# Performance work log

Hardware: AMD Instinct MI355X
Metric: run time of the kernel (lower is better)

Reference implementation:

```python
import jax, jax.numpy as jnp
import numpy as np

B, N, T, D, H = 64, 207, 24, 128, 8
DK = D // H
EPS = 1e-5


def setup_inputs() -> dict:
    key = jax.random.key(0)
    ks = jax.random.split(key, 18)
    s = 1.0 / np.sqrt(D)
    inp = {
        "hidden": jax.random.normal(ks[0], (B, N, T, D), jnp.float32),
        "matrix": jax.random.uniform(ks[1], (B, T, N, N), jnp.float32) / N,
        "Wq": jax.random.normal(ks[2], (D, D), jnp.float32) * s,
        "bq": jnp.zeros((D,), jnp.float32),
        "Wk": jax.random.normal(ks[3], (D, D), jnp.float32) * s,
        "bk": jnp.zeros((D,), jnp.float32),
        "Wv": jax.random.normal(ks[4], (D, D), jnp.float32) * s,
        "bv": jnp.zeros((D,), jnp.float32),
        "Wo": jax.random.normal(ks[5], (D, D), jnp.float32) * s,
        "bo": jnp.zeros((D,), jnp.float32),
        "Wgcn": jax.random.normal(ks[6], (D, D), jnp.float32) * s,
        "bgcn": jnp.zeros((D,), jnp.float32),
        "Wgate": jax.random.normal(ks[7], (D, 2 * D), jnp.float32) * (1.0 / np.sqrt(2 * D)),
        "bgate": jnp.zeros((D,), jnp.float32),
        "gamma": jnp.ones((D,), jnp.float32),
        "beta": jnp.zeros((D,), jnp.float32),
    }
    return inp


def reference(hidden, matrix, Wq, bq, Wk, bk, Wv, bv, Wo, bo,
              Wgcn, bgcn, Wgate, bgate, gamma, beta):
    # ---- GCN branch: per-timestep A·X then channel mixing (dmodel->dmodel)
    # hidden: [B,N,T,D], matrix: [B,T,N,N] -> aggregated [B,N,T,D]
    agg = jnp.einsum('bntc,btnm->bmtc', hidden, matrix)
    gcn_out = agg @ Wgcn.T + bgcn                       # [B,N,T,D]

    # ---- Causal multi-head temporal attention
    q = (hidden @ Wq.T + bq).reshape(B, N, T, H, DK)
    k = (hidden @ Wk.T + bk).reshape(B, N, T, H, DK)
    v = (hidden @ Wv.T + bv).reshape(B, N, T, H, DK)
    scale = 1.0 / np.sqrt(DK)
    scores = jnp.einsum('bnthe,bnshe->bnhts', q, k)     # [B,N,H,T,T]
    causal = jnp.triu(jnp.ones((T, T), bool), k=1)      # mask future
    scores = jnp.where(causal, -jnp.inf, scores)
    attn = jax.nn.softmax(scale * scores, axis=-1)
    ctx = jnp.einsum('bnhts,bnshd->bnthd', attn, v).reshape(B, N, T, D)
    attn_out = ctx @ Wo.T + bo                          # [B,N,T,D]

    # ---- Gated fusion: concat -> linear -> batchnorm (training stats) -> sigmoid
    gate_in = jnp.concatenate([gcn_out, attn_out], axis=-1)  # [B,N,T,2D]
    g = gate_in @ Wgate.T + bgate                            # [B,N,T,D]
    mean = jnp.mean(g, axis=(0, 1, 2))
    var = jnp.var(g, axis=(0, 1, 2))
    g = (g - mean) * jax.lax.rsqrt(var + EPS) * gamma + beta
    z = jax.nn.sigmoid(g)
    return z * gcn_out + (1.0 - z) * attn_out
```

## Files before the change

kernel.cpp:

```cpp
#include <hip/hip_runtime.h>

#define B_ 64
#define N_ 207
#define T_ 24
#define D_ 128
#define H_ 8
#define MROWS (B_*N_*T_)
#define SELEMS ((size_t)MROWS * D_)
#define NBLK_FB 768
#define BNROWS_FB 414
#define NBLK_FUSED (MROWS/128)
#define EPS_ 1e-5f

typedef __attribute__((ext_vector_type(8))) short s16x8;
typedef __attribute__((ext_vector_type(4))) float f32x4;

#define MFMA16(a,b,c) __builtin_amdgcn_mfma_f32_16x16x32_bf16(a,b,c,0,0,0)

__device__ __forceinline__ float bfu2f(unsigned short u) {
  return __uint_as_float(((unsigned int)u) << 16);
}
__device__ __forceinline__ unsigned short f2bfu(float f) {
  unsigned int x = __float_as_uint(f);
  return (unsigned short)((x + 0x7fffu + ((x >> 16) & 1u)) >> 16);
}
__device__ __forceinline__ unsigned int packbf2(float lo, float hi) {
  return (unsigned int)f2bfu(lo) | ((unsigned int)f2bfu(hi) << 16);
}

__global__ __launch_bounds__(256) void k_wcast(
    const float* __restrict__ Wq, const float* __restrict__ Wk,
    const float* __restrict__ Wv, const float* __restrict__ Wo,
    const float* __restrict__ Wgcn, const float* __restrict__ Wgate,
    unsigned short* __restrict__ out)
{
  const int idx4 = (blockIdx.x * 256 + threadIdx.x) * 4;
  if (idx4 >= 114688) return;
  const float* src; int off;
  if      (idx4 < 16384) { src = Wq;    off = idx4; }
  else if (idx4 < 32768) { src = Wk;    off = idx4 - 16384; }
  else if (idx4 < 49152) { src = Wv;    off = idx4 - 32768; }
  else if (idx4 < 65536) { src = Wo;    off = idx4 - 49152; }
  else if (idx4 < 81920) { src = Wgcn;  off = idx4 - 65536; }
  else                   { src = Wgate; off = idx4 - 81920; }
  const float4 v = *(const float4*)(src + off);
  ushort4 u;
  u.x = f2bfu(v.x); u.y = f2bfu(v.y); u.z = f2bfu(v.z); u.w = f2bfu(v.w);
  *(ushort4*)(out + idx4) = u;
}

__device__ __forceinline__ void gcn_load(
    const float* __restrict__ mbase, const float* __restrict__ hbase,
    int m0, int nn, int cb, int ch,
    float va[8], float vb[8], float ha[8], float hb[8])
{
  const int n_r0 = ch*32 + nn, n_r1 = n_r0 + 1;
  const bool rv0 = (n_r0 < N_), rv1 = (n_r1 < N_);
  const size_t nc0 = (size_t)(rv0 ? n_r0 : 0);
  const size_t nc1 = (size_t)(rv1 ? n_r1 : 0);
  {
    const float* r0 = mbase + nc0*N_ + m0 + cb;
    const float* r1 = mbase + nc1*N_ + m0 + cb;
    #pragma unroll
    for (int j = 0; j < 2; ++j) {
      const int mg = m0 + cb + j*4;
      if (mg + 3 < N_) {
        const float4 x0 = *(const float4*)(r0 + j*4);
        const float4 x1 = *(const float4*)(r1 + j*4);
        va[j*4+0]=x0.x; va[j*4+1]=x0.y; va[j*4+2]=x0.z; va[j*4+3]=x0.w;
        vb[j*4+0]=x1.x; vb[j*4+1]=x1.y; vb[j*4+2]=x1.z; vb[j*4+3]=x1.w;
      } else {
        #pragma unroll
        for (int e = 0; e < 4; ++e) {
          const bool ok = (mg + e) < N_;
          va[j*4+e] = ok ? r0[j*4+e] : 0.f;
          vb[j*4+e] = ok ? r1[j*4+e] : 0.f;
        }
      }
    }
    #pragma unroll
    for (int e = 0; e < 8; ++e) {
      if (!rv0) va[e] = 0.f;
      if (!rv1) vb[e] = 0.f;
    }
  }
  {
    const float* r0 = hbase + nc0*(T_*D_) + cb;
    const float* r1 = hbase + nc1*(T_*D_) + cb;
    const float4 x0a = *(const float4*)(r0);
    const float4 x0b = *(const float4*)(r0 + 4);
    const float4 x1a = *(const float4*)(r1);
    const float4 x1b = *(const float4*)(r1 + 4);
    ha[0]=x0a.x; ha[1]=x0a.y; ha[2]=x0a.z; ha[3]=x0a.w;
    ha[4]=x0b.x; ha[5]=x0b.y; ha[6]=x0b.z; ha[7]=x0b.w;
    hb[0]=x1a.x; hb[1]=x1a.y; hb[2]=x1a.z; hb[3]=x1a.w;
    hb[4]=x1b.x; hb[5]=x1b.y; hb[6]=x1b.z; hb[7]=x1b.w;
    #pragma unroll
    for (int e = 0; e < 8; ++e) {
      if (!rv0) ha[e] = 0.f;
      if (!rv1) hb[e] = 0.f;
    }
  }
}

__global__ __launch_bounds__(256) void k_gcn2(
    const float* __restrict__ hidden, const float* __restrict__ matrix,
    const unsigned short* __restrict__ Wgcnb, const float* __restrict__ bgcn,
    unsigned short* __restrict__ gcn)
{
  __shared__ __align__(16) unsigned char smem[40960];
  unsigned short* GsAll = (unsigned short*)smem;

  const int tid = threadIdx.x;
  const int w = tid >> 6, l = tid & 63;
  const int lr = l & 15, lg = l >> 4;
  const int m0 = blockIdx.x * 128;
  const int by = (int)blockIdx.y;
  const int b = by / T_, t = by % T_;

  const int nn = (tid & 15) * 2;
  const int cb = (tid >> 4) * 8;

  const float* mbase = matrix + (size_t)(b*T_ + t)*N_*N_;
  const float* hbase = hidden + (size_t)b*N_*T_*D_ + (size_t)t*D_;

  f32x4 acc1[2][8];
  #pragma unroll
  for (int mt = 0; mt < 2; mt++)
    #pragma unroll
    for (int nt = 0; nt < 8; nt++)
      #pragma unroll
      for (int e = 0; e < 4; e++) acc1[mt][nt][e] = 0.f;

  float va[8], vb[8], ha[8], hb[8];
  gcn_load(mbase, hbase, m0, nn, cb, 0, va, vb, ha, hb);

  #pragma unroll
  for (int ch = 0; ch < 7; ++ch) {
    unsigned char* base = smem + ((ch & 1) ? 20480 : 0);
    unsigned int* M32 = (unsigned int*)base;
    unsigned int* H32 = (unsigned int*)(base + 10240);
    #pragma unroll
    for (int e = 0; e < 8; ++e)
      M32[(cb + e)*20 + (tid & 15)] = packbf2(va[e], vb[e]);
    #pragma unroll
    for (int e = 0; e < 8; ++e)
      H32[(cb + e)*20 + (tid & 15)] = packbf2(ha[e], hb[e]);
    if (ch < 6)
      gcn_load(mbase, hbase, m0, nn, cb, ch + 1, va, vb, ha, hb);
    __syncthreads();
    const unsigned short* M16 = (const unsigned short*)M32;
    const unsigned short* H16 = (const unsigned short*)H32;
    const s16x8 af0 = *(const s16x8*)(M16 + (size_t)(w*32 +  0 + lr)*40 + lg*8);
    const s16x8 af1 = *(const s16x8*)(M16 + (size_t)(w*32 + 16 + lr)*40 + lg*8);
    #pragma unroll
    for (int nt = 0; nt < 8; ++nt) {
      const s16x8 bf = *(const s16x8*)(H16 + (size_t)(nt*16 + lr)*40 + lg*8);
      acc1[0][nt] = MFMA16(af0, bf, acc1[0][nt]);
      acc1[1][nt] = MFMA16(af1, bf, acc1[1][nt]);
    }
  }

  __syncthreads();
  unsigned short* gs = GsAll + (size_t)w * (32*136);
  #pragma unroll
  for (int nt = 0; nt < 8; nt++)
    #pragma unroll
    for (int mt = 0; mt < 2; mt++)
      #pragma unroll
      for (int r = 0; r < 4; r++)
        gs[(mt*16 + lg*4 + r)*136 + nt*16 + lr] = f2bfu(acc1[mt][nt][r]);

  f32x4 acc2[2][8];
  #pragma unroll
  for (int mt = 0; mt < 2; mt++)
    #pragma unroll
    for (int nt = 0; nt < 8; nt++)
      #pragma unroll
      for (int e = 0; e < 4; e++) acc2[mt][nt][e] = 0.f;

  #pragma unroll
  for (int ks = 0; ks < 4; ++ks) {
    const s16x8 a0 = *(const s16x8*)(gs + (size_t)( 0 + lr)*136 + ks*32 + lg*8);
    const s16x8 a1 = *(const s16x8*)(gs + (size_t)(16 + lr)*136 + ks*32 + lg*8);
    #pragma unroll
    for (int nt = 0; nt < 8; ++nt) {
      const s16x8 bf = *(const s16x8*)(Wgcnb + (size_t)(nt*16 + lr)*D_ + ks*32 + lg*8);
      acc2[0][nt] = MFMA16(a0, bf, acc2[0][nt]);
      acc2[1][nt] = MFMA16(a1, bf, acc2[1][nt]);
    }
  }

  #pragma unroll
  for (int nt = 0; nt < 8; nt++) {
    const float bsc = bgcn[nt*16 + lr];
    #pragma unroll
    for (int mt = 0; mt < 2; mt++)
      #pragma unroll
      for (int r = 0; r < 4; r++)
        gs[(mt*16 + lg*4 + r)*136 + nt*16 + lr] = f2bfu(acc2[mt][nt][r] + bsc);
  }
  const size_t Obase = ((size_t)b*N_ + (m0 + w*32))*(size_t)(T_*D_) + (size_t)t*D_;
  #pragma unroll
  for (int p = 0; p < 8; p++) {
    const int c = p*64 + l;
    const int row = c >> 4, c8 = (c & 15) * 8;
    const int gm = m0 + w*32 + row;
    if (gm < N_) {
      const s16x8 v = *(const s16x8*)(gs + row*136 + c8);
      *(s16x8*)(gcn + Obase + (size_t)row*(T_*D_) + c8) = v;
    }
  }
}

__global__ __launch_bounds__(256) void k_attn3(
    const float* __restrict__ hidden,
    const unsigned short* __restrict__ Wqb, const unsigned short* __restrict__ Wkb,
    const unsigned short* __restrict__ Wvb, const unsigned short* __restrict__ Wob,
    const float* __restrict__ bq, const float* __restrict__ bk,
    const float* __restrict__ bv, const float* __restrict__ bo,
    unsigned short* __restrict__ attnO)
{
  __shared__ __align__(16) unsigned short Xs[32*136], Qs[32*136],
                                          Ks[32*136], Vs[32*136];
  const int tid = threadIdx.x;
  const int w = tid >> 6, l = tid & 63;
  const int lr = l & 15, lg = l >> 4;
  const size_t bn = blockIdx.x;
  const float* X = hidden + bn * (size_t)(T_*D_);

  for (int i = tid; i < 32*16; i += 256) {
    const int row = i >> 4, g8 = (i & 15) * 8;
    s16x8 v;
    if (row < T_) {
      const float4 a  = *(const float4*)(X + (size_t)row*D_ + g8);
      const float4 b2 = *(const float4*)(X + (size_t)row*D_ + g8 + 4);
      v[0]=(short)f2bfu(a.x);  v[1]=(short)f2bfu(a.y);
      v[2]=(short)f2bfu(a.z);  v[3]=(short)f2bfu(a.w);
      v[4]=(short)f2bfu(b2.x); v[5]=(short)f2bfu(b2.y);
      v[6]=(short)f2bfu(b2.z); v[7]=(short)f2bfu(b2.w);
    } else {
      #pragma unroll
      for (int e = 0; e < 8; e++) v[e] = 0;
    }
    *(s16x8*)&Xs[row*136 + g8] = v;
  }
  __syncthreads();

  s16x8 af[2][4];
  #pragma unroll
  for (int mt = 0; mt < 2; mt++)
    #pragma unroll
    for (int ks = 0; ks < 4; ks++)
      af[mt][ks] = *(const s16x8*)&Xs[(mt*16 + lr)*136 + ks*32 + lg*8];

  const unsigned short* Wp[3] = {Wqb, Wkb, Wvb};
  const float*          bp[3] = {bq, bk, bv};
  unsigned short*       Op[3] = {Qs, Ks, Vs};
  #pragma unroll
  for (int o = 0; o < 3; o++) {
    f32x4 acc[2][2];
    #pragma unroll
    for (int mt = 0; mt < 2; mt++)
      #pragma unroll
      for (int nt = 0; nt < 2; nt++)
        #pragma unroll
        for (int e = 0; e < 4; e++) acc[mt][nt][e] = 0.f;
    #pragma unroll
    for (int ks = 0; ks < 4; ks++) {
      #pragma unroll
      for (int nt = 0; nt < 2; nt++) {
        const s16x8 bf = *(const s16x8*)(Wp[o] + (size_t)(w*32 + nt*16 + lr)*D_ + ks*32 + lg*8);
        acc[0][nt] = MFMA16(af[0][ks], bf, acc[0][nt]);
        acc[1][nt] = MFMA16(af[1][ks], bf, acc[1][nt]);
      }
    }
    #pragma unroll
    for (int nt = 0; nt < 2; nt++) {
      const float bb = bp[o][w*32 + nt*16 + lr];
      #pragma unroll
      for (int mt = 0; mt < 2; mt++)
        #pragma unroll
        for (int r = 0; r < 4; r++)
          Op[o][(mt*16 + lg*4 + r)*136 + w*32 + nt*16 + lr] =
              f2bfu(acc[mt][nt][r] + bb);
    }
  }
  __syncthreads();

  if (tid < H_*T_) {
    const int h = tid / T_, t = tid % T_;
    const int hb = h * 16;
    float q[16];
    {
      const s16x8 q0 = *(const s16x8*)&Qs[t*136 + hb];
      const s16x8 q1 = *(const s16x8*)&Qs[t*136 + hb + 8];
      #pragma unroll
      for (int e = 0; e < 8; e++) {
        q[e]   = bfu2f((unsigned short)q0[e]);
        q[8+e] = bfu2f((unsigned short)q1[e]);
      }
    }
    float p[T_];
    float mx = -1e30f;
    #pragma unroll
    for (int s = 0; s < T_; s++) {
      const s16x8 k0 = *(const s16x8*)&Ks[s*136 + hb];
      const s16x8 k1 = *(const s16x8*)&Ks[s*136 + hb + 8];
      float d = 0.f;
      #pragma unroll
      for (int e = 0; e < 8; e++) {
        d += q[e]   * bfu2f((unsigned short)k0[e]);
        d += q[8+e] * bfu2f((unsigned short)k1[e]);
      }
      d *= 0.25f;
      d = (s <= t) ? d : -1e30f;
      p[s] = d;
      mx = fmaxf(mx, d);
    }
    float den = 0.f;
    #pragma unroll
    for (int s = 0; s < T_; s++) {
      float e = __expf(p[s] - mx);
      e = (s <= t) ? e : 0.f;
      p[s] = e;
      den += e;
    }
    const float rd = 1.f / den;
    float o[16];
    #pragma unroll
    for (int e = 0; e < 16; e++) o[e] = 0.f;
    #pragma unroll
    for (int s = 0; s < T_; s++) {
      const float ps = p[s];
      const s16x8 v0 = *(const s16x8*)&Vs[s*136 + hb];
      const s16x8 v1 = *(const s16x8*)&Vs[s*136 + hb + 8];
      #pragma unroll
      for (int e = 0; e < 8; e++) {
        o[e]   += ps * bfu2f((unsigned short)v0[e]);
        o[8+e] += ps * bfu2f((unsigned short)v1[e]);
      }
    }
    s16x8 r0, r1;
    #pragma unroll
    for (int e = 0; e < 8; e++) {
      r0[e] = (short)f2bfu(o[e]   * rd);
      r1[e] = (short)f2bfu(o[8+e] * rd);
    }
    *(s16x8*)&Qs[t*136 + hb]     = r0;
    *(s16x8*)&Qs[t*136 + hb + 8] = r1;
  }
  __syncthreads();

  s16x8 cf[2][4];
  #pragma unroll
  for (int mt = 0; mt < 2; mt++)
    #pragma unroll
    for (int ks = 0; ks < 4; ks++)
      cf[mt][ks] = *(const s16x8*)&Qs[(mt*16 + lr)*136 + ks*32 + lg*8];
  f32x4 acc2[2][2];
  #pragma unroll
  for (int mt = 0; mt < 2; mt++)
    #pragma unroll
    for (int nt = 0; nt < 2; nt++)
      #pragma unroll
      for (int e = 0; e < 4; e++) acc2[mt][nt][e] = 0.f;
  #pragma unroll
  for (int ks = 0; ks < 4; ks++) {
    #pragma unroll
    for (int nt = 0; nt < 2; nt++) {
      const s16x8 bf = *(const s16x8*)(Wob + (size_t)(w*32 + nt*16 + lr)*D_ + ks*32 + lg*8);
      acc2[0][nt] = MFMA16(cf[0][ks], bf, acc2[0][nt]);
      acc2[1][nt] = MFMA16(cf[1][ks], bf, acc2[1][nt]);
    }
  }
  #pragma unroll
  for (int nt = 0; nt < 2; nt++) {
    const float bb = bo[w*32 + nt*16 + lr];
    #pragma unroll
    for (int mt = 0; mt < 2; mt++)
      #pragma unroll
      for (int r = 0; r < 4; r++)
        Xs[(mt*16 + lg*4 + r)*136 + w*32 + nt*16 + lr] =
            f2bfu(acc2[mt][nt][r] + bb);
  }
  __syncthreads();
  unsigned short* O = attnO + bn * (size_t)(T_*D_);
  for (int i = tid; i < 24*16; i += 256) {
    const int row = i >> 4, g8 = (i & 15) * 8;
    *(s16x8*)(O + (size_t)row*D_ + g8) = *(const s16x8*)&Xs[row*136 + g8];
  }
}

template<bool STATS>
__global__ __launch_bounds__(256) void k_gate(
    const unsigned short* __restrict__ A0, const unsigned short* __restrict__ A1,
    const unsigned short* __restrict__ Wb, const float* __restrict__ bias,
    float* __restrict__ Out, float* __restrict__ psum, float* __restrict__ psq)
{
  __shared__ float lbs[4*128], lbq[4*128];
  const int tid = threadIdx.x;
  const int w = tid >> 6, l = tid & 63;
  const int lr = l & 15, lg = l >> 4;
  const size_t m0 = (size_t)blockIdx.x * 128 + w * 32;

  f32x4 acc[2][8];
  #pragma unroll
  for (int mt = 0; mt < 2; mt++)
    #pragma unroll
    for (int nt = 0; nt < 8; nt++)
      #pragma unroll
      for (int e = 0; e < 4; e++) acc[mt][nt][e] = 0.f;

  #pragma unroll
  for (int ks = 0; ks < 8; ks++) {
    const unsigned short* Asrc = (ks >= 4) ? A1 : A0;
    const int kk = (ks >= 4) ? ks - 4 : ks;
    const s16x8 a0 = *(const s16x8*)(Asrc + (m0 +  0 + lr)*D_ + kk*32 + lg*8);
    const s16x8 a1 = *(const s16x8*)(Asrc + (m0 + 16 + lr)*D_ + kk*32 + lg*8);
    #pragma unroll
    for (int nt = 0; nt < 8; nt++) {
      const s16x8 bf = *(const s16x8*)(Wb + (size_t)(nt*16 + lr)*256 + ks*32 + lg*8);
      acc[0][nt] = MFMA16(a0, bf, acc[0][nt]);
      acc[1][nt] = MFMA16(a1, bf, acc[1][nt]);
    }
  }

  #pragma unroll
  for (int nt = 0; nt < 8; nt++) {
    const float b = bias[nt*16 + lr];
    float s = 0.f, q = 0.f;
    #pragma unroll
    for (int mt = 0; mt < 2; mt++)
      #pragma unroll
      for (int r = 0; r < 4; r++) {
        const float v = acc[mt][nt][r] + b;
        Out[(m0 + mt*16 + lg*4 + r)*D_ + nt*16 + lr] = v;
        if (STATS) { s += v; q += v*v; }
      }
    if (STATS) {
      s += __shfl_xor(s, 16); s += __shfl_xor(s, 32);
      q += __shfl_xor(q, 16); q += __shfl_xor(q, 32);
      if (lg == 0) {
        lbs[w*128 + nt*16 + lr] = s;
        lbq[w*128 + nt*16 + lr] = q;
      }
    }
  }
  if (STATS) {
    __syncthreads();
    if (tid < 128) {
      const float ss = lbs[tid] + lbs[128 + tid] + lbs[256 + tid] + lbs[384 + tid];
      const float qq = lbq[tid] + lbq[128 + tid] + lbq[256 + tid] + lbq[384 + tid];
      psum[(size_t)blockIdx.x*128 + tid] = ss;
      psq [(size_t)blockIdx.x*128 + tid] = qq;
    }
  }
}

__global__ __launch_bounds__(256) void k_bnstats(
    const float* __restrict__ g, float* __restrict__ psum, float* __restrict__ psq)
{
  const int tid = threadIdx.x;
  const int c4 = (tid & 31) * 4, sub = tid >> 5;
  const size_t r0 = (size_t)blockIdx.x * BNROWS_FB;
  float4 s = make_float4(0.f,0.f,0.f,0.f), q = make_float4(0.f,0.f,0.f,0.f);
  for (int i = sub; i < BNROWS_FB; i += 8) {
    const float4 x = *(const float4*)(g + (r0 + i)*D_ + c4);
    s.x += x.x; s.y += x.y; s.z += x.z; s.w += x.w;
    q.x += x.x*x.x; q.y += x.y*x.y; q.z += x.z*x.z; q.w += x.w*x.w;
  }
  __shared__ float ls[8*128], lq[8*128];
  *(float4*)&ls[sub*128 + c4] = s;
  *(float4*)&lq[sub*128 + c4] = q;
  __syncthreads();
  if (tid < 128) {
    float ss = 0.f, qq = 0.f;
    #pragma unroll
    for (int k = 0; k < 8; k++) { ss += ls[k*128 + tid]; qq += lq[k*128 + tid]; }
    psum[(size_t)blockIdx.x*128 + tid] = ss;
    psq [(size_t)blockIdx.x*128 + tid] = qq;
  }
}

__global__ __launch_bounds__(1024) void k_bnfinal(
    const float* __restrict__ psum, const float* __restrict__ psq, int nblk,
    float* __restrict__ meanv, float* __restrict__ invstdv)
{
  const int tid = threadIdx.x;
  const int sub = tid >> 7, ch = tid & 127;
  float s = 0.f, q = 0.f;
  for (int i = sub; i < nblk; i += 8) {
    s += psum[(size_t)i*128 + ch];
    q += psq [(size_t)i*128 + ch];
  }
  __shared__ float ls[8*128], lq[8*128];
  ls[sub*128 + ch] = s; lq[sub*128 + ch] = q;
  __syncthreads();
  if (tid < 128) {
    float ss = 0.f, qq = 0.f;
    #pragma unroll
    for (int k = 0; k < 8; k++) { ss += ls[k*128 + tid]; qq += lq[k*128 + tid]; }
    const float mean = ss / (float)MROWS;
    const float var  = qq / (float)MROWS - mean*mean;
    meanv[tid] = mean;
    invstdv[tid] = rsqrtf(var + EPS_);
  }
}

__global__ __launch_bounds__(256) void k_final(
    float* __restrict__ g,
    const unsigned short* __restrict__ gcn, const unsigned short* __restrict__ attn,
    const float* __restrict__ meanv, const float* __restrict__ invstdv,
    const float* __restrict__ gamma, const float* __restrict__ beta)
{
  const size_t tot4 = SELEMS >> 2;
  for (size_t i4 = (size_t)blockIdx.x*blockDim.x + threadIdx.x; i4 < tot4;
       i4 += (size_t)gridDim.x*blockDim.x) {
    const int c4 = (int)(i4 & 31) * 4;
    const float4 gv = ((const float4*)g)[i4];
    const ushort4 gc = ((const ushort4*)gcn)[i4];
    const ushort4 at = ((const ushort4*)attn)[i4];
    const float4 m4 = *(const float4*)(meanv + c4);
    const float4 s4 = *(const float4*)(invstdv + c4);
    const float4 ga = *(const float4*)(gamma + c4);
    const float4 be = *(const float4*)(beta + c4);
    float4 outv;
    { const float y = (gv.x - m4.x)*s4.x*ga.x + be.x;
      const float z = 1.f/(1.f + __expf(-y));
      outv.x = z*bfu2f(gc.x) + (1.f - z)*bfu2f(at.x); }
    { const float y = (gv.y - m4.y)*s4.y*ga.y + be.y;
      const float z = 1.f/(1.f + __expf(-y));
      outv.y = z*bfu2f(gc.y) + (1.f - z)*bfu2f(at.y); }
    { const float y = (gv.z - m4.z)*s4.z*ga.z + be.z;
      const float z = 1.f/(1.f + __expf(-y));
      outv.z = z*bfu2f(gc.z) + (1.f - z)*bfu2f(at.z); }
    { const float y = (gv.w - m4.w)*s4.w*ga.w + be.w;
      const float z = 1.f/(1.f + __expf(-y));
      outv.w = z*bfu2f(gc.w) + (1.f - z)*bfu2f(at.w); }
    ((float4*)g)[i4] = outv;
  }
}

extern "C" void kernel_launch(void* const* d_in, const int* in_sizes, int n_in,
                              void* d_out, int out_size, void* d_ws, size_t ws_size,
                              hipStream_t stream)
{
  (void)in_sizes; (void)n_in; (void)out_size;
  const float* hidden = (const float*)d_in[0];
  const float* matrix = (const float*)d_in[1];
  const float* Wq   = (const float*)d_in[2];  const float* bq    = (const float*)d_in[3];
  const float* Wk   = (const float*)d_in[4];  const float* bk    = (const float*)d_in[5];
  const float* Wv   = (const float*)d_in[6];  const float* bv    = (const float*)d_in[7];
  const float* Wo   = (const float*)d_in[8];  const float* bo    = (const float*)d_in[9];
  const float* Wgcn = (const float*)d_in[10]; const float* bgcn  = (const float*)d_in[11];
  const float* Wgate= (const float*)d_in[12]; const float* bgate = (const float*)d_in[13];
  const float* gamma= (const float*)d_in[14]; const float* beta  = (const float*)d_in[15];
  float* out = (float*)d_out;

  unsigned short* WB = (unsigned short*)d_ws;
  unsigned short* Wqb    = WB;
  unsigned short* Wkb    = WB + 16384;
  unsigned short* Wvb    = WB + 32768;
  unsigned short* Wob    = WB + 49152;
  unsigned short* Wgcnb  = WB + 65536;
  unsigned short* Wgateb = WB + 81920;
  unsigned short* X1     = WB + 114688;
  unsigned short* X2     = X1 + SELEMS;
  float* psum    = (float*)(X2 + SELEMS);

  const size_t base_bytes = (size_t)(WB + 114688 - (unsigned short*)d_ws)*2
                          + 2*SELEMS*2;
  const size_t fused_bytes = base_bytes + ((size_t)NBLK_FUSED*128*2 + 256)*4;
  const bool fused = (ws_size >= fused_bytes);
  const int nblk = fused ? NBLK_FUSED : NBLK_FB;
  float* psq     = psum + (size_t)nblk*128;
  float* meanv   = psq  + (size_t)nblk*128;
  float* invstdv = meanv + 128;

  k_wcast<<<112, 256, 0, stream>>>(Wq, Wk, Wv, Wo, Wgcn, Wgate, WB);
  k_gcn2 <<<dim3(2, B_*T_), 256, 0, stream>>>(hidden, matrix, Wgcnb, bgcn, X2);
  k_attn3<<<B_*N_, 256, 0, stream>>>(hidden, Wqb, Wkb, Wvb, Wob,
                                     bq, bk, bv, bo, X1);
  if (fused) {
    k_gate<true><<<MROWS/128, 256, 0, stream>>>(X2, X1, Wgateb, bgate, out, psum, psq);
  } else {
    k_gate<false><<<MROWS/128, 256, 0, stream>>>(X2, X1, Wgateb, bgate, out, psum, psq);
    k_bnstats<<<NBLK_FB, 256, 0, stream>>>(out, psum, psq);
  }
  k_bnfinal<<<1, 1024, 0, stream>>>(psum, psq, nblk, meanv, invstdv);
  k_final<<<2048, 256, 0, stream>>>(out, X2, X1, meanv, invstdv, gamma, beta);
}
```

Baseline: 815.6 us.

## Compute causal attention scores and PV with per-wave MFMA instead of scalar loops

Replaces the scalar per-thread attention (192 threads each looping over 24 keys) with MFMA tiles. Each wave computes QK^T and P·V for the two heads whose columns it produced in the projection, so no block barrier is needed between projection and attention. V is stored transposed in shared memory and the probabilities are staged in a per-wave buffer as bf16. The softmax now skips max subtraction and rounds probabilities to bf16, which trades some numerical robustness for speed.

New measurement: 750.9 us. -7.9%, faster.

```diff
diff --git a/kernel.cpp b/kernel.cpp
--- a/kernel.cpp
+++ b/kernel.cpp
@@ -221,8 +221,11 @@
     const float* __restrict__ bv, const float* __restrict__ bo,
     unsigned short* __restrict__ attnO)
 {
-  __shared__ __align__(16) unsigned short Xs[32*136], Qs[32*136],
-                                          Ks[32*136], Vs[32*136];
+  __shared__ __align__(16) unsigned short Xs[32*136];
+  __shared__ __align__(16) unsigned short Qs[32*136];
+  __shared__ __align__(16) unsigned short Ks[32*136];
+  __shared__ __align__(16) unsigned short Vt[128*40];
+  __shared__ __align__(16) unsigned short Ps[4][32*40];
   const int tid = threadIdx.x;
   const int w = tid >> 6, l = tid & 63;
   const int lr = l & 15, lg = l >> 4;
@@ -253,10 +256,10 @@
     #pragma unroll
     for (int ks = 0; ks < 4; ks++)
       af[mt][ks] = *(const s16x8*)&Xs[(mt*16 + lr)*136 + ks*32 + lg*8];
+  __syncthreads();
 
   const unsigned short* Wp[3] = {Wqb, Wkb, Wvb};
   const float*          bp[3] = {bq, bk, bv};
-  unsigned short*       Op[3] = {Qs, Ks, Vs};
   #pragma unroll
   for (int o = 0; o < 3; o++) {
     f32x4 acc[2][2];
@@ -281,83 +284,90 @@
       #pragma unroll
       for (int mt = 0; mt < 2; mt++)
         #pragma unroll
-        for (int r = 0; r < 4; r++)
-          Op[o][(mt*16 + lg*4 + r)*136 + w*32 + nt*16 + lr] =
-              f2bfu(acc[mt][nt][r] + bb);
-    }
+        for (int r = 0; r < 4; r++) {
+          const unsigned short hv = f2bfu(acc[mt][nt][r] + bb);
+          const int trow = mt*16 + lg*4 + r;
+          const int dcol = w*32 + nt*16 + lr;
+          if (o == 0)      Qs[trow*136 + dcol] = hv;
+          else if (o == 1) Ks[trow*136 + dcol] = hv;
+          else             Vt[dcol*40 + trow] = hv;
+        }
+    }
+  }
+
+  unsigned short* Pw = Ps[w];
+  #pragma unroll
+  for (int hi = 0; hi < 2; hi++) {
+    const int hh = 2*w + hi;
+    s16x8 zv;
+    #pragma unroll
+    for (int e = 0; e < 8; e++) zv[e] = 0;
+    s16x8 aq[2], bkf[2];
+    #pragma unroll
+    for (int mt = 0; mt < 2; mt++) {
+      s16x8 tv = zv;
+      if (lg < 2) tv = *(const s16x8*)&Qs[(mt*16 + lr)*136 + hh*16 + lg*8];
+      aq[mt] = tv;
+    }
+    #pragma unroll
+    for (int nt = 0; nt < 2; nt++) {
+      s16x8 tv = zv;
+      if (lg < 2) tv = *(const s16x8*)&Ks[(nt*16 + lr)*136 + hh*16 + lg*8];
+      bkf[nt] = tv;
+    }
+    f32x4 accS[2][2];
+    #pragma unroll
+    for (int mt = 0; mt < 2; mt++)
+      #pragma unroll
+      for (int nt = 0; nt < 2; nt++) {
+        f32x4 z4; z4[0]=0.f; z4[1]=0.f; z4[2]=0.f; z4[3]=0.f;
+        accS[mt][nt] = MFMA16(aq[mt], bkf[nt], z4);
+      }
+    #pragma unroll
+    for (int mt = 0; mt < 2; mt++) {
+      #pragma unroll
+      for (int r = 0; r < 4; r++) {
+        const int t = mt*16 + lg*4 + r;
+        const bool m0 = (lr <= t), m1 = (16 + lr <= t);
+        float e0 = m0 ? __expf(0.25f * accS[mt][0][r]) : 0.f;
+        float e1 = m1 ? __expf(0.25f * accS[mt][1][r]) : 0.f;
+        float den = e0 + e1;
+        den += __shfl_xor(den, 1);
+        den += __shfl_xor(den, 2);
+        den += __shfl_xor(den, 4);
+        den += __shfl_xor(den, 8);
+        const float rd = 1.f / den;
+        Pw[t*40 + lr]      = f2bfu(e0 * rd);
+        Pw[t*40 + 16 + lr] = f2bfu(e1 * rd);
+      }
+    }
+    s16x8 ap[2];
+    #pragma unroll
+    for (int mt = 0; mt < 2; mt++)
+      ap[mt] = *(const s16x8*)&Pw[(mt*16 + lr)*40 + lg*8];
+    const s16x8 bvf = *(const s16x8*)&Vt[(hh*16 + lr)*40 + lg*8];
+    f32x4 accP[2];
+    #pragma unroll
+    for (int mt = 0; mt < 2; mt++) {
+      f32x4 z4; z4[0]=0.f; z4[1]=0.f; z4[2]=0.f; z4[3]=0.f;
+      accP[mt] = MFMA16(ap[mt], bvf, z4);
+    }
+    #pragma unroll
+    for (int mt = 0; mt < 2; mt++)
+      #pragma unroll
+      for (int r = 0; r < 4; r++) {
+        const int t = mt*16 + lg*4 + r;
+        if (t < T_) Xs[t*136 + hh*16 + lr] = f2bfu(accP[mt][r]);
+      }
   }
   __syncthreads();
 
-  if (tid < H_*T_) {
-    const int h = tid / T_, t = tid % T_;
-    const int hb = h * 16;
-    float q[16];
-    {
-      const s16x8 q0 = *(const s16x8*)&Qs[t*136 + hb];
-      const s16x8 q1 = *(const s16x8*)&Qs[t*136 + hb + 8];
-      #pragma unroll
-      for (int e = 0; e < 8; e++) {
-        q[e]   = bfu2f((unsigned short)q0[e]);
-        q[8+e] = bfu2f((unsigned short)q1[e]);
-      }
-    }
-    float p[T_];
-    float mx = -1e30f;
-    #pragma unroll
-    for (int s = 0; s < T_; s++) {
-      const s16x8 k0 = *(const s16x8*)&Ks[s*136 + hb];
-      const s16x8 k1 = *(const s16x8*)&Ks[s*136 + hb + 8];
-      float d = 0.f;
-      #pragma unroll
-      for (int e = 0; e < 8; e++) {
-        d += q[e]   * bfu2f((unsigned short)k0[e]);
-        d += q[8+e] * bfu2f((unsigned short)k1[e]);
-      }
-      d *= 0.25f;
-      d = (s <= t) ? d : -1e30f;
-      p[s] = d;
-      mx = fmaxf(mx, d);
-    }
-    float den = 0.f;
-    #pragma unroll
-    for (int s = 0; s < T_; s++) {
-      float e = __expf(p[s] - mx);
-      e = (s <= t) ? e : 0.f;
-      p[s] = e;
-      den += e;
-    }
-    const float rd = 1.f / den;
-    float o[16];
-    #pragma unroll
-    for (int e = 0; e < 16; e++) o[e] = 0.f;
-    #pragma unroll
-    for (int s = 0; s < T_; s++) {
-      const float ps = p[s];
-      const s16x8 v0 = *(const s16x8*)&Vs[s*136 + hb];
-      const s16x8 v1 = *(const s16x8*)&Vs[s*136 + hb + 8];
-      #pragma unroll
-      for (int e = 0; e < 8; e++) {
-        o[e]   += ps * bfu2f((unsigned short)v0[e]);
-        o[8+e] += ps * bfu2f((unsigned short)v1[e]);
-      }
-    }
-    s16x8 r0, r1;
-    #pragma unroll
-    for (int e = 0; e < 8; e++) {
-      r0[e] = (short)f2bfu(o[e]   * rd);
-      r1[e] = (short)f2bfu(o[8+e] * rd);
-    }
-    *(s16x8*)&Qs[t*136 + hb]     = r0;
-    *(s16x8*)&Qs[t*136 + hb + 8] = r1;
-  }
-  __syncthreads();
-
   s16x8 cf[2][4];
   #pragma unroll
   for (int mt = 0; mt < 2; mt++)
     #pragma unroll
     for (int ks = 0; ks < 4; ks++)
-      cf[mt][ks] = *(const s16x8*)&Qs[(mt*16 + lr)*136 + ks*32 + lg*8];
+      cf[mt][ks] = *(const s16x8*)&Xs[(mt*16 + lr)*136 + ks*32 + lg*8];
   f32x4 acc2[2][2];
   #pragma unroll
   for (int mt = 0; mt < 2; mt++)
@@ -381,14 +391,14 @@
     for (int mt = 0; mt < 2; mt++)
       #pragma unroll
       for (int r = 0; r < 4; r++)
-        Xs[(mt*16 + lg*4 + r)*136 + w*32 + nt*16 + lr] =
+        Qs[(mt*16 + lg*4 + r)*136 + w*32 + nt*16 + lr] =
             f2bfu(acc2[mt][nt][r] + bb);
   }
   __syncthreads();
   unsigned short* O = attnO + bn * (size_t)(T_*D_);
   for (int i = tid; i < 24*16; i += 256) {
     const int row = i >> 4, g8 = (i & 15) * 8;
-    *(s16x8*)(O + (size_t)row*D_ + g8) = *(const s16x8*)&Xs[row*136 + g8];
+    *(s16x8*)(O + (size_t)row*D_ + g8) = *(const s16x8*)&Qs[row*136 + g8];
   }
 }
 
```
